# Kernel optimization log

Hardware: AMD Instinct MI355X
Metric: run time of the kernel (lower is better)

The kernel has to match this reference:

```python
import jax, jax.numpy as jnp
import numpy as np

B = 2_000_000
IN, HID = 5, 4


def setup_inputs() -> dict:
    key = jax.random.key(0)
    ks = jax.random.split(key, 16)
    f = lambda k, shp: (jax.random.normal(k, shp, dtype=jnp.float32) * 0.3)
    inp = {
        "xl": jax.random.normal(ks[0], (B, IN), dtype=jnp.float32),
        "yl": jax.random.normal(ks[1], (B, IN), dtype=jnp.float32),
        "xr": jax.random.normal(ks[2], (B, IN), dtype=jnp.float32),
        "yr": jax.random.normal(ks[3], (B, IN), dtype=jnp.float32),
        # 6 stacked branches, order: [lxl, lyl, lxr, lyr, rxl, ryl]
        "W1": f(ks[4], (6, HID, IN)),
        "b1": f(ks[5], (6, HID)),
        "W2": f(ks[6], (6, HID, HID)),
        "b2": f(ks[7], (6, HID)),
        # fc3 with 2 outputs, order: [lxl, lyl, rxl, ryl] (branch idx 0,1,4,5)
        "W3_2": f(ks[8], (4, 2, HID)),
        "b3_2": f(ks[9], (4, 2)),
        # fc3 with 1 output, order: [lxr, lyr] (branch idx 2,3)
        "W3_1": f(ks[10], (2, 1, HID)),
        "b3_1": f(ks[11], (2, 1)),
        # fc4, order: [xl, yl]
        "W4": f(ks[12], (2, 1, HID)),
        "b4": f(ks[13], (2, 1)),
    }
    return inp


def reference(xl, yl, xr, yr, W1, b1, W2, b2, W3_2, b3_2, W3_1, b3_1, W4, b4):
    # Stack the six branch inputs: [6, B, 5]. NOTE: fc_1lyr consumes yl (yr unused),
    # faithful to the original forward.
    X = jnp.stack([xl, yl, xr, yl, xl, yl], axis=0)
    h1 = jax.nn.sigmoid(jnp.einsum("kbi,khi->kbh", X, W1) + b1[:, None, :])
    h2 = jax.nn.sigmoid(jnp.einsum("kbh,kgh->kbg", h1, W2) + b2[:, None, :])
    # fc3 heads with 2 outputs: branches lxl(0), lyl(1), rxl(4), ryl(5)
    h2_2 = h2[jnp.array([0, 1, 4, 5])]                       # [4, B, 4]
    o2 = jnp.einsum("kbh,koh->kbo", h2_2, W3_2) + b3_2[:, None, :]  # [4, B, 2]
    # fc3 heads with 1 output: branches lxr(2), lyr(3)
    h2_1 = h2[jnp.array([2, 3])]                             # [2, B, 4]
    o1 = jnp.einsum("kbh,koh->kbo", h2_1, W3_1) + b3_1[:, None, :]  # [2, B, 1]
    # concat (per-sample dim, was dim=0 unbatched)
    out_xl = jnp.concatenate([o2[0], o2[2]], axis=-1)        # [B, 4]
    out_yl = jnp.concatenate([o2[1], o2[3]], axis=-1)        # [B, 4]
    fc4xl = out_xl @ W4[0].T + b4[0]                         # [B, 1]
    fc4yl = out_yl @ W4[1].T + b4[1]                         # [B, 1]
    out = jnp.concatenate([o1[0], o1[1], fc4xl, fc4yl], axis=-1)  # [B, 4]
    return out
```

## Files before the change

kernel.cpp:

```cpp
#include <hip/hip_runtime.h>

#define NT 256

typedef float f32x2 __attribute__((ext_vector_type(2)));
typedef float f32x4u __attribute__((ext_vector_type(4), aligned(8)));
typedef float f32x2u __attribute__((ext_vector_type(2), aligned(8)));

#if defined(__has_builtin)
#if __has_builtin(__builtin_amdgcn_exp2f)
#define EXP2F __builtin_amdgcn_exp2f
#else
#define EXP2F exp2f
#endif
#else
#define EXP2F exp2f
#endif

__device__ __forceinline__ f32x2 bc2(float w) {
    f32x2 r; r.x = w; r.y = w; return r;
}
__device__ __forceinline__ f32x2 pfma(f32x2 a, f32x2 b, f32x2 c) {
    return __builtin_elementwise_fma(a, b, c);
}

#define WS_W1 0
#define WS_B1 120
#define WS_W2 144
#define WS_B2 240
#define WS_FW 264
#define WS_FB 288

__global__ void mlp6_prefold(const float* __restrict__ W1, const float* __restrict__ b1,
                             const float* __restrict__ W2, const float* __restrict__ b2,
                             const float* __restrict__ W3_2, const float* __restrict__ b3_2,
                             const float* __restrict__ W3_1, const float* __restrict__ b3_1,
                             const float* __restrict__ W4, const float* __restrict__ b4,
                             float* __restrict__ ws)
{
    const float C = -1.442695040888963f;
    int t = threadIdx.x;
    if (t < 120) {
        ws[WS_W1 + t] = C * W1[t];
    } else if (t < 144) {
        ws[WS_B1 + (t - 120)] = C * b1[t - 120];
    } else if (t < 240) {
        ws[WS_W2 + (t - 144)] = C * W2[t - 144];
    } else if (t < 264) {
        ws[WS_B2 + (t - 240)] = C * b2[t - 240];
    } else if (t < 288) {
        int q = t - 264, k = q >> 2, h = q & 3;
        float v;
        if (k == 0)      v = W4[0]*W3_2[h]      + W4[1]*W3_2[4 + h];
        else if (k == 1) v = W4[4]*W3_2[8 + h]  + W4[5]*W3_2[12 + h];
        else if (k == 2) v = W3_1[h];
        else if (k == 3) v = W3_1[4 + h];
        else if (k == 4) v = W4[2]*W3_2[16 + h] + W4[3]*W3_2[20 + h];
        else             v = W4[6]*W3_2[24 + h] + W4[7]*W3_2[28 + h];
        ws[WS_FW + q] = v;
    } else if (t < 292) {
        int j = t - 288;
        float v;
        if (j == 0)      v = b3_1[0];
        else if (j == 1) v = b3_1[1];
        else if (j == 2) v = W4[0]*b3_2[0] + W4[1]*b3_2[1] + W4[2]*b3_2[4] + W4[3]*b3_2[5] + b4[0];
        else             v = W4[4]*b3_2[2] + W4[5]*b3_2[3] + W4[6]*b3_2[6] + W4[7]*b3_2[7] + b4[1];
        ws[WS_FB + j] = v;
    }
}

__device__ __forceinline__ f32x2 sig2(f32x2 v) {
    f32x2 e;
    e.x = EXP2F(v.x);
    e.y = EXP2F(v.y);
    f32x2 d = e + bc2(1.0f);
    f32x2 r;
    r.x = __builtin_amdgcn_rcpf(d.x);
    r.y = __builtin_amdgcn_rcpf(d.y);
    return r;
}

__device__ __forceinline__ void load10(const float* base, float f[10]) {
    const char* p = (const char*)base;
    f32x4u a = *(const f32x4u*)(p);
    f32x4u b = *(const f32x4u*)(p + 16);
    f32x2u c = *(const f32x2u*)(p + 32);
    f[0] = a.x; f[1] = a.y; f[2] = a.z; f[3] = a.w;
    f[4] = b.x; f[5] = b.y; f[6] = b.z; f[7] = b.w;
    f[8] = c.x; f[9] = c.y;
}

__global__ __launch_bounds__(NT, 3)
void mlp6_fused(const float* __restrict__ xl,
                const float* __restrict__ yl,
                const float* __restrict__ xr,
                const float* __restrict__ ws,
                float* __restrict__ out, int nq)
{
    int gq = blockIdx.x * NT + threadIdx.x;
    if (gq >= nq) gq = nq - 1;

    float LA[10], LB[10], LC[10];
    load10(xl + (long long)gq * 10, LA);
    load10(yl + (long long)gq * 10, LB);
    load10(xr + (long long)gq * 10, LC);

    f32x2 xp[5], yp[5], cp[5];
    #pragma unroll
    for (int q = 0; q < 5; q++) {
        xp[q].x = LA[q]; xp[q].y = LA[5 + q];
        yp[q].x = LB[q]; yp[q].y = LB[5 + q];
        cp[q].x = LC[q]; cp[q].y = LC[5 + q];
    }

    const float* wW1 = ws + WS_W1;
    const float* wb1 = ws + WS_B1;
    const float* wW2 = ws + WS_W2;
    const float* wb2 = ws + WS_B2;
    const float* wfw = ws + WS_FW;
    const float* wfb = ws + WS_FB;

    f32x2 o0 = bc2(wfb[0]), o1 = bc2(wfb[1]), o2 = bc2(wfb[2]), o3 = bc2(wfb[3]);

    auto pair2 = [&](int kA, const f32x2 (&inA)[5], f32x2& oA,
                     int kB, const f32x2 (&inB)[5], f32x2& oB) {
        f32x2 hA[4], hB[4];
        #pragma unroll
        for (int hh = 0; hh < 4; hh++) {
            f32x2 aA = pfma(inA[0], bc2(wW1[kA*20 + hh*5]), bc2(wb1[kA*4 + hh]));
            f32x2 aB = pfma(inB[0], bc2(wW1[kB*20 + hh*5]), bc2(wb1[kB*4 + hh]));
            #pragma unroll
            for (int q = 1; q < 5; q++) {
                aA = pfma(inA[q], bc2(wW1[kA*20 + hh*5 + q]), aA);
                aB = pfma(inB[q], bc2(wW1[kB*20 + hh*5 + q]), aB);
            }
            hA[hh] = sig2(aA);
            hB[hh] = sig2(aB);
        }
        f32x2 cA[4], cB[4];
        #pragma unroll
        for (int g = 0; g < 4; g++) {
            f32x2 aA = pfma(hA[0], bc2(wW2[kA*16 + g*4]), bc2(wb2[kA*4 + g]));
            f32x2 aB = pfma(hB[0], bc2(wW2[kB*16 + g*4]), bc2(wb2[kB*4 + g]));
            #pragma unroll
            for (int q = 1; q < 4; q++) {
                aA = pfma(hA[q], bc2(wW2[kA*16 + g*4 + q]), aA);
                aB = pfma(hB[q], bc2(wW2[kB*16 + g*4 + q]), aB);
            }
            cA[g] = sig2(aA);
            cB[g] = sig2(aB);
        }
        #pragma unroll
        for (int g = 0; g < 4; g++) {
            oA = pfma(cA[g], bc2(wfw[kA*4 + g]), oA);
            oB = pfma(cB[g], bc2(wfw[kB*4 + g]), oB);
        }
    };

    pair2(0, xp, o2, 1, yp, o3);
    pair2(4, xp, o2, 3, yp, o1);
    pair2(5, yp, o3, 2, cp, o0);

    float4 r0, r1;
    r0.x = o0.x; r0.y = o1.x; r0.z = o2.x; r0.w = o3.x;
    r1.x = o0.y; r1.y = o1.y; r1.z = o2.y; r1.w = o3.y;
    float4* out4 = (float4*)out;
    out4[(long long)gq * 2]     = r0;
    out4[(long long)gq * 2 + 1] = r1;
}

extern "C" void kernel_launch(void* const* d_in, const int* in_sizes, int n_in,
                              void* d_out, int out_size, void* d_ws, size_t ws_size,
                              hipStream_t stream) {
    const float* xl   = (const float*)d_in[0];
    const float* yl   = (const float*)d_in[1];
    const float* xr   = (const float*)d_in[2];
    const float* W1   = (const float*)d_in[4];
    const float* b1   = (const float*)d_in[5];
    const float* W2   = (const float*)d_in[6];
    const float* b2   = (const float*)d_in[7];
    const float* W3_2 = (const float*)d_in[8];
    const float* b3_2 = (const float*)d_in[9];
    const float* W3_1 = (const float*)d_in[10];
    const float* b3_1 = (const float*)d_in[11];
    const float* W4   = (const float*)d_in[12];
    const float* b4   = (const float*)d_in[13];
    float* out = (float*)d_out;
    float* ws  = (float*)d_ws;

    mlp6_prefold<<<1, 320, 0, stream>>>(
        W1, b1, W2, b2, W3_2, b3_2, W3_1, b3_1, W4, b4, ws);

    int B  = in_sizes[0] / 5;
    int nq = B >> 1;
    int blocks = (nq + NT - 1) / NT;
    mlp6_fused<<<blocks, NT, 0, stream>>>(xl, yl, xr, ws, out, nq);
}
```

Measured before the change: 39.36 us.

## Process two sample-pairs per thread and prefetch second pair's inputs during compute

Each thread now handles two pairs of samples, one from each half of the batch. It issues the second pair's input loads in stages, interleaved with the first pair's compute, so memory latency overlaps with math. The grid is halved and the launch bounds hint drops from 3 to 2 waves per SIMD, leaving more registers for the extra live inputs. Input loads change from 16/8-byte chunks to five 8-byte loads each, with a repack of the lanes. The cost is higher register pressure and less occupancy-based latency hiding.

Result: no change. 38.95 us (-1.0%).

```diff
diff --git a/kernel.cpp b/kernel.cpp
--- a/kernel.cpp
+++ b/kernel.cpp
@@ -3,8 +3,7 @@
 #define NT 256
 
 typedef float f32x2 __attribute__((ext_vector_type(2)));
-typedef float f32x4u __attribute__((ext_vector_type(4), aligned(8)));
-typedef float f32x2u __attribute__((ext_vector_type(2), aligned(8)));
+typedef float f32x4 __attribute__((ext_vector_type(4)));
 
 #if defined(__has_builtin)
 #if __has_builtin(__builtin_amdgcn_exp2f)
@@ -79,38 +78,26 @@
     return r;
 }
 
-__device__ __forceinline__ void load10(const float* base, float f[10]) {
-    const char* p = (const char*)base;
-    f32x4u a = *(const f32x4u*)(p);
-    f32x4u b = *(const f32x4u*)(p + 16);
-    f32x2u c = *(const f32x2u*)(p + 32);
-    f[0] = a.x; f[1] = a.y; f[2] = a.z; f[3] = a.w;
-    f[4] = b.x; f[5] = b.y; f[6] = b.z; f[7] = b.w;
-    f[8] = c.x; f[9] = c.y;
-}
-
-__global__ __launch_bounds__(NT, 3)
+__device__ __forceinline__ void repack5(const f32x2 L[5], f32x2 p[5]) {
+    p[0].x = L[0].x; p[0].y = L[2].y;
+    p[1].x = L[0].y; p[1].y = L[3].x;
+    p[2].x = L[1].x; p[2].y = L[3].y;
+    p[3].x = L[1].y; p[3].y = L[4].x;
+    p[4].x = L[2].x; p[4].y = L[4].y;
+}
+
+__global__ __launch_bounds__(NT, 2)
 void mlp6_fused(const float* __restrict__ xl,
                 const float* __restrict__ yl,
                 const float* __restrict__ xr,
                 const float* __restrict__ ws,
-                float* __restrict__ out, int nq)
+                float* __restrict__ out, int nq, int nqh)
 {
-    int gq = blockIdx.x * NT + threadIdx.x;
-    if (gq >= nq) gq = nq - 1;
-
-    float LA[10], LB[10], LC[10];
-    load10(xl + (long long)gq * 10, LA);
-    load10(yl + (long long)gq * 10, LB);
-    load10(xr + (long long)gq * 10, LC);
-
-    f32x2 xp[5], yp[5], cp[5];
-    #pragma unroll
-    for (int q = 0; q < 5; q++) {
-        xp[q].x = LA[q]; xp[q].y = LA[5 + q];
-        yp[q].x = LB[q]; yp[q].y = LB[5 + q];
-        cp[q].x = LC[q]; cp[q].y = LC[5 + q];
-    }
+    int t = blockIdx.x * NT + threadIdx.x;
+    if (t >= nqh) t = nqh - 1;
+    int g0 = t;
+    int g1 = t + nqh;
+    if (g1 >= nq) g1 = nq - 1;
 
     const float* wW1 = ws + WS_W1;
     const float* wb1 = ws + WS_B1;
@@ -118,8 +105,6 @@
     const float* wb2 = ws + WS_B2;
     const float* wfw = ws + WS_FW;
     const float* wfb = ws + WS_FB;
-
-    f32x2 o0 = bc2(wfb[0]), o1 = bc2(wfb[1]), o2 = bc2(wfb[2]), o3 = bc2(wfb[3]);
 
     auto pair2 = [&](int kA, const f32x2 (&inA)[5], f32x2& oA,
                      int kB, const f32x2 (&inB)[5], f32x2& oB) {
@@ -156,16 +141,67 @@
         }
     };
 
+    const f32x2* x0 = (const f32x2*)xl + (long long)g0 * 5;
+    const f32x2* y0 = (const f32x2*)yl + (long long)g0 * 5;
+    const f32x2* c0 = (const f32x2*)xr + (long long)g0 * 5;
+    const f32x2* x1 = (const f32x2*)xl + (long long)g1 * 5;
+    const f32x2* y1 = (const f32x2*)yl + (long long)g1 * 5;
+    const f32x2* c1 = (const f32x2*)xr + (long long)g1 * 5;
+
+    f32x2 LA0[5], LB0[5], LC0[5];
+    #pragma unroll
+    for (int q = 0; q < 5; q++) LA0[q] = x0[q];
+    #pragma unroll
+    for (int q = 0; q < 5; q++) LB0[q] = y0[q];
+    #pragma unroll
+    for (int q = 0; q < 5; q++) LC0[q] = c0[q];
+    f32x2 LA1[5];
+    #pragma unroll
+    for (int q = 0; q < 5; q++) LA1[q] = x1[q];
+
+    f32x2 xp[5], yp[5], cp[5];
+    repack5(LA0, xp);
+    repack5(LB0, yp);
+    repack5(LC0, cp);
+
+    f32x2 o0 = bc2(wfb[0]), o1 = bc2(wfb[1]), o2 = bc2(wfb[2]), o3 = bc2(wfb[3]);
+
     pair2(0, xp, o2, 1, yp, o3);
+    f32x2 LB1[5];
+    #pragma unroll
+    for (int q = 0; q < 5; q++) LB1[q] = y1[q];
     pair2(4, xp, o2, 3, yp, o1);
+    f32x2 LC1[5];
+    #pragma unroll
+    for (int q = 0; q < 5; q++) LC1[q] = c1[q];
     pair2(5, yp, o3, 2, cp, o0);
 
-    float4 r0, r1;
-    r0.x = o0.x; r0.y = o1.x; r0.z = o2.x; r0.w = o3.x;
-    r1.x = o0.y; r1.y = o1.y; r1.z = o2.y; r1.w = o3.y;
-    float4* out4 = (float4*)out;
-    out4[(long long)gq * 2]     = r0;
-    out4[(long long)gq * 2 + 1] = r1;
+    {
+        f32x4 r0, r1;
+        r0.x = o0.x; r0.y = o1.x; r0.z = o2.x; r0.w = o3.x;
+        r1.x = o0.y; r1.y = o1.y; r1.z = o2.y; r1.w = o3.y;
+        f32x4* o4 = (f32x4*)out + (long long)g0 * 2;
+        o4[0] = r0;
+        o4[1] = r1;
+    }
+
+    repack5(LA1, xp);
+    repack5(LB1, yp);
+    repack5(LC1, cp);
+
+    f32x2 p0 = bc2(wfb[0]), p1 = bc2(wfb[1]), p2 = bc2(wfb[2]), p3 = bc2(wfb[3]);
+    pair2(0, xp, p2, 1, yp, p3);
+    pair2(4, xp, p2, 3, yp, p1);
+    pair2(5, yp, p3, 2, cp, p0);
+
+    {
+        f32x4 r0, r1;
+        r0.x = p0.x; r0.y = p1.x; r0.z = p2.x; r0.w = p3.x;
+        r1.x = p0.y; r1.y = p1.y; r1.z = p2.y; r1.w = p3.y;
+        f32x4* o4 = (f32x4*)out + (long long)g1 * 2;
+        o4[0] = r0;
+        o4[1] = r1;
+    }
 }
 
 extern "C" void kernel_launch(void* const* d_in, const int* in_sizes, int n_in,
@@ -190,8 +226,9 @@
     mlp6_prefold<<<1, 320, 0, stream>>>(
         W1, b1, W2, b2, W3_2, b3_2, W3_1, b3_1, W4, b4, ws);
 
-    int B  = in_sizes[0] / 5;
-    int nq = B >> 1;
-    int blocks = (nq + NT - 1) / NT;
-    mlp6_fused<<<blocks, NT, 0, stream>>>(xl, yl, xr, ws, out, nq);
-}
+    int B   = in_sizes[0] / 5;
+    int nq  = B >> 1;
+    int nqh = (nq + 1) >> 1;
+    int blocks = (nqh + NT - 1) / NT;
+    mlp6_fused<<<blocks, NT, 0, stream>>>(xl, yl, xr, ws, out, nq, nqh);
+}
```
